# Performance work log

Measured on AMD Instinct MI355X. Metric: run time of the kernel, lower is better.

## Reference

```python
import jax, jax.numpy as jnp
import numpy as np

HEADS = 4
DIM_HEAD = 128


def setup_inputs() -> dict:
    key = jax.random.key(0)
    k1, k2, k3 = jax.random.split(key, 3)
    dim = 256
    hidden = HEADS * DIM_HEAD  # 512
    x = jax.random.normal(k1, (16, dim, 64, 64), dtype=jnp.float32)
    # 1x1 conv weights stored as [out_ch, in_ch] (kernel dims squeezed)
    w_qkv = jax.random.normal(k2, (hidden * 3, dim), dtype=jnp.float32) * (1.0 / np.sqrt(dim))
    w_out = jax.random.normal(k3, (dim, hidden), dtype=jnp.float32) * (1.0 / np.sqrt(hidden))
    b_out = jnp.zeros((dim,), dtype=jnp.float32)
    return {"x": x, "w_qkv": w_qkv, "w_out": w_out, "b_out": b_out}


def reference(x, w_qkv, w_out, b_out):
    b, c, h, w = x.shape
    n = h * w
    # 1x1 conv == per-pixel linear projection
    qkv = jnp.einsum('bchw,oc->bohw', x, w_qkv)           # [b, 3*heads*dh, h, w]
    qkv = qkv.reshape(b, 3, HEADS, DIM_HEAD, n)           # 'b (qkv heads c) h w -> qkv b heads c (h w)'
    q, k, v = qkv[:, 0], qkv[:, 1], qkv[:, 2]             # [b, heads, dh, n]
    k = jax.nn.softmax(k, axis=-1)                        # softmax over spatial positions
    context = jnp.einsum('bhdn,bhen->bhde', k, v)         # [b, heads, dh, dh]
    out = jnp.einsum('bhde,bhdn->bhen', context, q)       # [b, heads, dh, n]
    out = out.reshape(b, HEADS * DIM_HEAD, h, w)          # 'b heads c (h w) -> b (heads c) h w'
    y = jnp.einsum('bchw,oc->bohw', out, w_out) + b_out[None, :, None, None]
    return y
```

## Files before the change

kernel.cpp:

```cpp
#include <hip/hip_runtime.h>

#define BATCH 16
#define CIN   256
#define NSP   4096
#define HID   512

typedef short v8s __attribute__((ext_vector_type(8)));
typedef float v4f __attribute__((ext_vector_type(4)));

__device__ __forceinline__ unsigned short f2bf(float f) {
    union { float f; unsigned u; } a; a.f = f;
    unsigned r = a.u + 0x7fffu + ((a.u >> 16) & 1u);
    return (unsigned short)(r >> 16);
}

__device__ __forceinline__ void gld_lds16(const unsigned short* g, unsigned short* l) {
    __builtin_amdgcn_global_load_lds(
        (const __attribute__((address_space(1))) unsigned int*)g,
        (__attribute__((address_space(3))) unsigned int*)l,
        16, 0, 0);
}


__global__ __launch_bounds__(256) void k_prep(const float* __restrict__ x,
                                              const float* __restrict__ wq,
                                              unsigned short* __restrict__ xbf,
                                              unsigned short* __restrict__ xT,
                                              unsigned short* __restrict__ wbf,
                                              unsigned short* __restrict__ wqT,
                                              float* __restrict__ zacc) {
    const int bid = blockIdx.x;
    const int t = threadIdx.x;
    if (bid >= 4320) {
        zacc[(bid - 4320) * 256 + t] = 0.f;
        return;
    }
    if (bid >= 4096) {
        const int wid = bid - 4096;
        if (wid < 192) {
            const int g = wid * 256 + t;
            const float4 f0 = *(const float4*)(wq + (size_t)g * 8);
            const float4 f1 = *(const float4*)(wq + (size_t)g * 8 + 4);
            union { unsigned short s[8]; uint4 u; } p;
            p.s[0] = f2bf(f0.x); p.s[1] = f2bf(f0.y); p.s[2] = f2bf(f0.z); p.s[3] = f2bf(f0.w);
            p.s[4] = f2bf(f1.x); p.s[5] = f2bf(f1.y); p.s[6] = f2bf(f1.z); p.s[7] = f2bf(f1.w);
            *(uint4*)(wbf + (size_t)g * 8) = p.u;
            return;
        }
        __shared__ float tile[64 * 65];
        const int bb = wid - 192;
        const int u0 = (bb & 7) * 64, c0 = (bb >> 3) * 64;
        {
            const int cl = (t & 15) * 4, ul = t >> 4;
            #pragma unroll
            for (int i = 0; i < 4; i++) {
                int u = ul + i * 16;
                const float4 f = *(const float4*)(wq + (size_t)(u0 + u) * CIN + c0 + cl);
                *(float4*)(&tile[u * 65 + cl]) = f;
            }
        }
        __syncthreads();
        {
            const int ul4 = (t & 15) * 4, cl = t >> 4;
            #pragma unroll
            for (int i = 0; i < 4; i++) {
                int c = cl + i * 16;
                union { unsigned short s[4]; uint2 u; } p;
                #pragma unroll
                for (int j = 0; j < 4; j++)
                    p.s[j] = f2bf(tile[(ul4 + j) * 65 + c]);
                *(uint2*)(wqT + (size_t)(c0 + c) * HID + u0 + ul4) = p.u;
            }
        }
        return;
    }
    __shared__ float tile[64 * 65];
    const int n0 = (bid & 63) * 64, c0 = ((bid >> 6) & 3) * 64, bz = bid >> 8;
    const float* xb = x + (size_t)bz * CIN * NSP;
    {
        const int nl = (t & 15) * 4, cl = t >> 4;
        #pragma unroll
        for (int i = 0; i < 4; i++) {
            int c = cl + i * 16;
            const float4 f = *(const float4*)(xb + (size_t)(c0 + c) * NSP + n0 + nl);
            *(float4*)(&tile[c * 65 + nl]) = f;
            union { unsigned short s[4]; uint2 u; } p;
            p.s[0] = f2bf(f.x); p.s[1] = f2bf(f.y); p.s[2] = f2bf(f.z); p.s[3] = f2bf(f.w);
            *(uint2*)(xbf + ((size_t)bz * CIN + c0 + c) * NSP + n0 + nl) = p.u;
        }
    }
    __syncthreads();
    {
        const int cl4 = (t & 15) * 4, nl = t >> 4;
        #pragma unroll
        for (int i = 0; i < 4; i++) {
            int n = nl + i * 16;
            union { unsigned short s[4]; uint2 u; } p;
            #pragma unroll
            for (int j = 0; j < 4; j++)
                p.s[j] = f2bf(tile[(cl4 + j) * 65 + n]);
            *(uint2*)(xT + ((size_t)bz * NSP + n0 + n) * CIN + c0 + cl4) = p.u;
        }
    }
}

__global__ __launch_bounds__(256, 2) void k_ks(const unsigned short* __restrict__ wbf,
                                               const unsigned short* __restrict__ xT,
                                               const unsigned short* __restrict__ xbf,
                                               float* __restrict__ Sp,
                                               float* __restrict__ zacc) {
    __shared__ __align__(16) unsigned short A1s[4][64][64];
    __shared__ __align__(16) unsigned short A2s[256][64];
    __shared__ __align__(16) unsigned short Es[64][64];

    const int t = threadIdx.x;
    const int id = blockIdx.x;
    const int bz = id & 15, dblk = (id >> 4) & 7, nc = id >> 7;
    const int d0 = dblk * 64;
    const int nbase = nc * 1024;
    const int lane = t & 63, wv = t >> 6, quad = lane >> 4, l15 = lane & 15;
    const int srow8 = lane >> 3, sslot = lane & 7;
    const int scol = ((sslot - srow8) & 7) * 8;
    const int sw0 = ((quad + l15) & 7) * 8;
    const int wc = wv;

    auto STAGE_A1 = [&](int n0s) {
        #pragma unroll
        for (int i = 0; i < 8; i++) {
            const int flat = wv * 8 + i;
            const int kl = flat >> 3, rb = flat & 7;
            gld_lds16(xT + ((size_t)bz * NSP + n0s + rb * 8 + srow8) * CIN + kl * 64 + scol,
                      &A1s[kl][rb * 8][0]);
        }
    };
    auto STAGE_A2 = [&](int n0s) {
        #pragma unroll
        for (int i = 0; i < 8; i++) {
            const int rb = wv * 8 + i;
            gld_lds16(xbf + ((size_t)bz * CIN + rb * 8 + srow8) * NSP + n0s + scol,
                      &A2s[rb * 8][0]);
        }
    };

    {
        #pragma unroll
        for (int i = 0; i < 8; i++) {
            const int flat = wv * 8 + i;
            const int kk = flat >> 3, rb = flat & 7;
            gld_lds16(wbf + (size_t)(512 + d0 + rb * 8 + srow8) * CIN + kk * 64 + scol,
                      &A2s[0][0] + (kk * 64 + rb * 8) * 64);
        }
    }
    __syncthreads();
    v8s Wkf[4][4][2];
    #pragma unroll
    for (int kk = 0; kk < 4; kk++)
        #pragma unroll
        for (int ni = 0; ni < 4; ni++)
            #pragma unroll
            for (int h = 0; h < 2; h++) {
                union { v8s v; uint4 u; } rr;
                rr.u = *(const uint4*)(&A2s[0][0] +
                        (size_t)(kk * 64 + ni * 16 + l15) * 64 + (sw0 ^ (h * 32)));
                Wkf[kk][ni][h] = rr.v;
            }
    __syncthreads();

    v4f acc2[4][4];
    #pragma unroll
    for (int i = 0; i < 4; i++)
        #pragma unroll
        for (int j = 0; j < 4; j++) acc2[i][j] = (v4f)0.f;
    float za[4] = {0.f, 0.f, 0.f, 0.f};

    STAGE_A1(nbase);

    for (int nt = 0; nt < 16; nt++) {
        const int n0s = nbase + nt * 64;
        __syncthreads();
        STAGE_A2(n0s);

        v4f acc1[4];
        #pragma unroll
        for (int i = 0; i < 4; i++) acc1[i] = (v4f)0.f;

        __builtin_amdgcn_s_setprio(1);
        #pragma unroll
        for (int kk = 0; kk < 4; kk++) {
            #pragma unroll
            for (int h = 0; h < 2; h++) {
                union { v8s v; uint4 u; } rr;
                rr.u = *(const uint4*)(&A1s[kk][wv * 16 + l15][0] + (sw0 ^ (h * 32)));
                const v8s af = rr.v;
                #pragma unroll
                for (int ni = 0; ni < 4; ni++)
                    acc1[ni] = __builtin_amdgcn_mfma_f32_16x16x32_bf16(af, Wkf[kk][ni][h], acc1[ni], 0, 0, 0);
            }
        }
        __builtin_amdgcn_s_setprio(0);

        #pragma unroll
        for (int ni = 0; ni < 4; ni++) {
            const int d = ni * 16 + l15;
            union { unsigned short s[4]; uint2 u; } p;
            #pragma unroll
            for (int rr = 0; rr < 4; rr++) {
                float e = __expf(acc1[ni][rr]);
                za[ni] += e;
                p.s[rr] = f2bf(e);
            }
            const int slot = (wv * 2 + (quad >> 1) + d) & 7;
            *(uint2*)(&Es[d][slot * 8 + (quad & 1) * 4]) = p.u;
        }
        __syncthreads();
        if (nt < 15) STAGE_A1(n0s + 64);

        __builtin_amdgcn_s_setprio(1);
        #pragma unroll
        for (int kst = 0; kst < 2; kst++) {
            const int esw = sw0 ^ (kst * 32);
            v8s af[4], bfr[4];
            #pragma unroll
            for (int mi = 0; mi < 4; mi++) {
                union { v8s v; uint4 u; } rr;
                rr.u = *(const uint4*)(&A2s[wc * 64 + mi * 16 + l15][0] + esw);
                af[mi] = rr.v;
            }
            #pragma unroll
            for (int ni = 0; ni < 4; ni++) {
                union { v8s v; uint4 u; } rr;
                rr.u = *(const uint4*)(&Es[ni * 16 + l15][0] + esw);
                bfr[ni] = rr.v;
            }
            #pragma unroll
            for (int mi = 0; mi < 4; mi++)
                #pragma unroll
                for (int ni = 0; ni < 4; ni++)
                    acc2[mi][ni] = __builtin_amdgcn_mfma_f32_16x16x32_bf16(af[mi], bfr[ni], acc2[mi][ni], 0, 0, 0);
        }
        __builtin_amdgcn_s_setprio(0);
    }

    #pragma unroll
    for (int ni = 0; ni < 4; ni++) {
        float z = za[ni];
        z += __shfl_xor(z, 16);
        z += __shfl_xor(z, 32);
        if (quad == 0)
            atomicAdd(&zacc[bz * 512 + d0 + ni * 16 + l15], z);
    }

    const int bh = bz * 4 + (dblk >> 1);
    const int ch = wc >> 1;
    float* outp = Sp + ((size_t)(bh * 2 + ch) * 4 + nc) * 16384;
    #pragma unroll
    for (int ni = 0; ni < 4; ni++) {
        const int dl = (dblk & 1) * 64 + ni * 16 + l15;
        #pragma unroll
        for (int mi = 0; mi < 4; mi++) {
            const int cl = (wc & 1) * 64 + mi * 16 + quad * 4;
            *(v4f*)(outp + dl * 128 + cl) = acc2[mi][ni];
        }
    }
}

__global__ __launch_bounds__(256) void k_sred(const float* __restrict__ Sp,
                                              unsigned short* __restrict__ Sred) {
    const int qv = blockIdx.x * 256 + threadIdx.x;
    const int bh = qv >> 13, r = qv & 8191;
    const int dl = r >> 6, cq6 = r & 63;
    const int ch = cq6 >> 5, clq = cq6 & 31;
    const float* p = Sp + ((size_t)(bh * 2 + ch) * 4) * 16384 + dl * 128 + clq * 4;
    float4 s = *(const float4*)p;
    #pragma unroll
    for (int kc = 1; kc < 4; kc++) {
        const float4 f = *(const float4*)(p + (size_t)kc * 16384);
        s.x += f.x; s.y += f.y; s.z += f.z; s.w += f.w;
    }
    union { unsigned short us[4]; uint2 u; } pk;
    pk.us[0] = f2bf(s.x); pk.us[1] = f2bf(s.y); pk.us[2] = f2bf(s.z); pk.us[3] = f2bf(s.w);
    *(uint2*)(Sred + (size_t)bh * 32768 + dl * 256 + cq6 * 4) = pk.u;
}

__global__ __launch_bounds__(256) void k_redwc(const unsigned short* __restrict__ Sred,
                                               const float* __restrict__ zacc,
                                               const unsigned short* __restrict__ wbf,
                                               const float* __restrict__ w_out,
                                               unsigned short* __restrict__ Wc) {
    __shared__ unsigned short Ds[128 * 136];
    __shared__ float zinv[128];
    const int t = threadIdx.x;
    const int bh = blockIdx.x;  const int b = bh >> 2, h = bh & 3;
    const int lane = t & 63, wv = t >> 6, quad = lane >> 4, l15 = lane & 15;

    if (t < 128) zinv[t] = 1.0f / zacc[b * 512 + h * 128 + t];
    __syncthreads();

    {
        const int wm = (wv & 1) * 64, wn = (wv >> 1) * 64;
        const unsigned short* Sb = Sred + (size_t)bh * 32768;
        const unsigned short* Vb = wbf + (size_t)(1024 + h * 128) * CIN;
        v4f acc[4][4];
        #pragma unroll
        for (int i = 0; i < 4; i++)
            #pragma unroll
            for (int j = 0; j < 4; j++) acc[i][j] = (v4f)0.f;
        for (int kk = 0; kk < CIN; kk += 32) {
            v8s af[4], bfr[4];
            #pragma unroll
            for (int mi = 0; mi < 4; mi++) {
                union { v8s v; uint4 u; } rr;
                rr.u = *(const uint4*)(Sb + (size_t)(wm + mi * 16 + l15) * 256 + kk + quad * 8);
                af[mi] = rr.v;
            }
            #pragma unroll
            for (int ni = 0; ni < 4; ni++) {
                union { v8s v; uint4 u; } rr;
                rr.u = *(const uint4*)(Vb + (size_t)(wn + ni * 16 + l15) * 256 + kk + quad * 8);
                bfr[ni] = rr.v;
            }
            #pragma unroll
            for (int mi = 0; mi < 4; mi++)
                #pragma unroll
                for (int ni = 0; ni < 4; ni++)
                    acc[mi][ni] = __builtin_amdgcn_mfma_f32_16x16x32_bf16(af[mi], bfr[ni], acc[mi][ni], 0, 0, 0);
        }
        float zq[4][4];
        #pragma unroll
        for (int mi = 0; mi < 4; mi++)
            #pragma unroll
            for (int rr = 0; rr < 4; rr++)
                zq[mi][rr] = zinv[wm + mi * 16 + quad * 4 + rr];
        #pragma unroll
        for (int mi = 0; mi < 4; mi++)
            #pragma unroll
            for (int ni = 0; ni < 4; ni++)
                #pragma unroll
                for (int rr = 0; rr < 4; rr++)
                    Ds[(wm + mi * 16 + quad * 4 + rr) * 136 + wn + ni * 16 + l15] =
                        f2bf(acc[mi][ni][rr] * zq[mi][rr]);
    }
    __syncthreads();

    {
        const int wm = wv * 64;
        v4f acc[4][8];
        #pragma unroll
        for (int i = 0; i < 4; i++)
            #pragma unroll
            for (int j = 0; j < 8; j++) acc[i][j] = (v4f)0.f;
        for (int kk = 0; kk < 128; kk += 32) {
            v8s af[4], bfr[8];
            #pragma unroll
            for (int mi = 0; mi < 4; mi++) {
                int o = wm + mi * 16 + l15;
                const float* wp = w_out + (size_t)o * HID + h * 128 + kk + quad * 8;
                float4 f0 = *(const float4*)wp;
                float4 f1 = *(const float4*)(wp + 4);
                union { v8s v; unsigned short s[8]; } r;
                r.s[0] = f2bf(f0.x); r.s[1] = f2bf(f0.y); r.s[2] = f2bf(f0.z); r.s[3] = f2bf(f0.w);
                r.s[4] = f2bf(f1.x); r.s[5] = f2bf(f1.y); r.s[6] = f2bf(f1.z); r.s[7] = f2bf(f1.w);
                af[mi] = r.v;
            }
            #pragma unroll
            for (int ni = 0; ni < 8; ni++) {
                union { v8s v; uint4 u; } r;
                r.u = *(const uint4*)(&Ds[(ni * 16 + l15) * 136 + kk + quad * 8]);
                bfr[ni] = r.v;
            }
            #pragma unroll
            for (int mi = 0; mi < 4; mi++)
                #pragma unroll
                for (int ni = 0; ni < 8; ni++)
                    acc[mi][ni] = __builtin_amdgcn_mfma_f32_16x16x32_bf16(af[mi], bfr[ni], acc[mi][ni], 0, 0, 0);
        }
        #pragma unroll
        for (int ni = 0; ni < 8; ni++) {
            int d = ni * 16 + l15;
            #pragma unroll
            for (int mi = 0; mi < 4; mi++)
                #pragma unroll
                for (int rr = 0; rr < 4; rr++) {
                    int o = wm + mi * 16 + quad * 4 + rr;
                    Wc[((size_t)b * 256 + o) * HID + h * 128 + d] = f2bf(acc[mi][ni][rr]);
                }
        }
    }
}

__global__ __launch_bounds__(256) void k_chain(const unsigned short* __restrict__ Wc,
                                               const unsigned short* __restrict__ wqT,
                                               unsigned short* __restrict__ Weff) {
    __shared__ __align__(16) unsigned short As[128 * 64];
    __shared__ __align__(16) unsigned short Bs[128 * 64];
    const int t = threadIdx.x;
    const int c0 = blockIdx.x * 128, o0 = blockIdx.y * 128, bz = blockIdx.z;
    const int lane = t & 63, wv = t >> 6, quad = lane >> 4, l15 = lane & 15;
    const int wmC = (wv & 1) * 64, wnO = (wv >> 1) * 64;

    const int srow8 = lane >> 3, sslot = lane & 7;
    const int scol = ((sslot - srow8) & 7) * 8;
    const int sw0 = ((quad + l15) & 7) * 8;

    const unsigned short* Ag = wqT + (size_t)(c0 + wv * 32 + srow8) * HID + scol;
    const unsigned short* Bg = Wc + ((size_t)bz * 256 + o0 + wv * 32 + srow8) * HID + scol;
    unsigned short* Al = As + wv * 32 * 64;
    unsigned short* Bl = Bs + wv * 32 * 64;

    v4f acc[4][4];
    #pragma unroll
    for (int i = 0; i < 4; i++)
        #pragma unroll
        for (int j = 0; j < 4; j++) acc[i][j] = (v4f)0.f;

    for (int kk = 0; kk < HID; kk += 64) {
        #pragma unroll
        for (int cc = 0; cc < 4; cc++) {
            gld_lds16(Ag + (size_t)(cc * 8) * HID + kk, Al + cc * 8 * 64);
            gld_lds16(Bg + (size_t)(cc * 8) * HID + kk, Bl + cc * 8 * 64);
        }
        __syncthreads();
        #pragma unroll
        for (int h = 0; h < 2; h++) {
            const int sw = sw0 ^ (h * 32);
            v8s af[4], bfr[4];
            #pragma unroll
            for (int mi = 0; mi < 4; mi++) {
                union { v8s v; uint4 u; } rr;
                rr.u = *(const uint4*)(&As[(wmC + mi * 16 + l15) * 64 + sw]);
                af[mi] = rr.v;
            }
            #pragma unroll
            for (int ni = 0; ni < 4; ni++) {
                union { v8s v; uint4 u; } rr;
                rr.u = *(const uint4*)(&Bs[(wnO + ni * 16 + l15) * 64 + sw]);
                bfr[ni] = rr.v;
            }
            #pragma unroll
            for (int mi = 0; mi < 4; mi++)
                #pragma unroll
                for (int ni = 0; ni < 4; ni++)
                    acc[mi][ni] = __builtin_amdgcn_mfma_f32_16x16x32_bf16(af[mi], bfr[ni], acc[mi][ni], 0, 0, 0);
        }
        __syncthreads();
    }
    #pragma unroll
    for (int ni = 0; ni < 4; ni++) {
        const int o = o0 + wnO + ni * 16 + l15;
        #pragma unroll
        for (int mi = 0; mi < 4; mi++) {
            const int c = c0 + wmC + mi * 16 + quad * 4;
            union { unsigned short s[4]; uint2 u; } p;
            #pragma unroll
            for (int rr = 0; rr < 4; rr++) p.s[rr] = f2bf(acc[mi][ni][rr]);
            *(uint2*)(Weff + ((size_t)bz * 256 + o) * 256 + c) = p.u;
        }
    }
}

__global__ __launch_bounds__(256) void k_y(const unsigned short* __restrict__ Weff,
                                           const unsigned short* __restrict__ xT,
                                           const float* __restrict__ b_out,
                                           float* __restrict__ y) {
    __shared__ __align__(16) unsigned short As[128 * 64];
    __shared__ __align__(16) unsigned short Bs[128 * 64];
    const int t = threadIdx.x;
    const int o0 = blockIdx.x * 128;
    const int n0 = blockIdx.y * 128;
    const int bz = blockIdx.z;
    const int lane = t & 63, wv = t >> 6, quad = lane >> 4, l15 = lane & 15;
    const int wmN = (wv & 1) * 64, wnO = (wv >> 1) * 64;

    const int srow8 = lane >> 3, sslot = lane & 7;
    const int scol = ((sslot - srow8) & 7) * 8;
    const int sw0 = ((quad + l15) & 7) * 8;

    const unsigned short* Ag = xT + ((size_t)bz * NSP + n0 + wv * 32 + srow8) * CIN + scol;
    const unsigned short* Bg = Weff + ((size_t)bz * 256 + o0 + wv * 32 + srow8) * CIN + scol;
    unsigned short* Al = As + wv * 32 * 64;
    unsigned short* Bl = Bs + wv * 32 * 64;

    v4f acc[4][4];
    #pragma unroll
    for (int i = 0; i < 4; i++)
        #pragma unroll
        for (int j = 0; j < 4; j++) acc[i][j] = (v4f)0.f;

    for (int kk = 0; kk < CIN; kk += 64) {
        #pragma unroll
        for (int cc = 0; cc < 4; cc++) {
            gld_lds16(Ag + (size_t)(cc * 8) * CIN + kk, Al + cc * 8 * 64);
            gld_lds16(Bg + (size_t)(cc * 8) * CIN + kk, Bl + cc * 8 * 64);
        }
        __syncthreads();
        #pragma unroll
        for (int h = 0; h < 2; h++) {
            const int sw = sw0 ^ (h * 32);
            v8s af[4], bfr[4];
            #pragma unroll
            for (int mi = 0; mi < 4; mi++) {
                union { v8s v; uint4 u; } rr;
                rr.u = *(const uint4*)(&As[(wmN + mi * 16 + l15) * 64 + sw]);
                af[mi] = rr.v;
            }
            #pragma unroll
            for (int ni = 0; ni < 4; ni++) {
                union { v8s v; uint4 u; } rr;
                rr.u = *(const uint4*)(&Bs[(wnO + ni * 16 + l15) * 64 + sw]);
                bfr[ni] = rr.v;
            }
            #pragma unroll
            for (int mi = 0; mi < 4; mi++)
                #pragma unroll
                for (int ni = 0; ni < 4; ni++)
                    acc[mi][ni] = __builtin_amdgcn_mfma_f32_16x16x32_bf16(af[mi], bfr[ni], acc[mi][ni], 0, 0, 0);
        }
        __syncthreads();
    }
    #pragma unroll
    for (int ni = 0; ni < 4; ni++) {
        const int o = o0 + wnO + ni * 16 + l15;
        const float bias = b_out[o];
        #pragma unroll
        for (int mi = 0; mi < 4; mi++) {
            const int n = n0 + wmN + mi * 16 + quad * 4;
            v4f v = acc[mi][ni];
            v[0] += bias; v[1] += bias; v[2] += bias; v[3] += bias;
            *(v4f*)(y + ((size_t)bz * 256 + o) * NSP + n) = v;
        }
    }
}

extern "C" void kernel_launch(void* const* d_in, const int* in_sizes, int n_in,
                              void* d_out, int out_size, void* d_ws, size_t ws_size,
                              hipStream_t stream) {
    (void)in_sizes; (void)n_in; (void)out_size; (void)ws_size;
    const float* x     = (const float*)d_in[0];
    const float* w_qkv = (const float*)d_in[1];
    const float* w_out = (const float*)d_in[2];
    const float* b_out = (const float*)d_in[3];
    float* y = (float*)d_out;
    char* ws = (char*)d_ws;

    unsigned short* xT   = (unsigned short*)(ws);
    unsigned short* xbf  = (unsigned short*)(ws + 33554432);
    float*          Sp   = (float*)(ws + 67108864);
    float*          zacc = (float*)(ws + 100663296);
    unsigned short* Sred = (unsigned short*)(ws + 100696064);
    unsigned short* Wc   = (unsigned short*)(ws + 104890368);
    unsigned short* Weff = (unsigned short*)(ws + 109084672);
    unsigned short* wbf  = (unsigned short*)(ws + 111181824);
    unsigned short* wqT  = (unsigned short*)(ws + 111968256);

    k_prep <<<dim3(4352),       256, 0, stream>>>(x, w_qkv, xbf, xT, wbf, wqT, zacc);
    k_ks   <<<dim3(512),        256, 0, stream>>>(wbf, xT, xbf, Sp, zacc);
    k_sred <<<dim3(2048),       256, 0, stream>>>(Sp, Sred);
    k_redwc<<<dim3(64),         256, 0, stream>>>(Sred, zacc, wbf, w_out, Wc);
    k_chain<<<dim3(2, 2, 16),   256, 0, stream>>>(Wc, wqT, Weff);
    k_y    <<<dim3(2, 32, 16),  256, 0, stream>>>(Weff, xT, b_out, y);
}
```

Measured before the change: 229.4 us.

## Double-buffer LDS tiles and load x operand directly from global into registers

The k_ks kernel now double-buffers the xT tile in LDS and the exp(K) tile, prefetching the next A1 tile at the top of each iteration so one barrier per iteration suffices instead of two. The A2 (xbf) operand is no longer staged through LDS; each lane loads its MFMA fragments directly from global memory into registers. The K-weight fragments are also read straight from global memory instead of through LDS. This cuts barriers and LDS traffic, but it adds global-load latency on the critical path before the second MFMA stage, and the direct loads may be less coalesced.

```diff
diff --git a/kernel.cpp b/kernel.cpp
--- a/kernel.cpp
+++ b/kernel.cpp
@@ -109,9 +109,8 @@
                                                const unsigned short* __restrict__ xbf,
                                                float* __restrict__ Sp,
                                                float* __restrict__ zacc) {
-    __shared__ __align__(16) unsigned short A1s[4][64][64];
-    __shared__ __align__(16) unsigned short A2s[256][64];
-    __shared__ __align__(16) unsigned short Es[64][64];
+    __shared__ __align__(16) unsigned short A1s[2][4][64][64];
+    __shared__ __align__(16) unsigned short Es[2][64][64];
 
     const int t = threadIdx.x;
     const int id = blockIdx.x;
@@ -124,34 +123,16 @@
     const int sw0 = ((quad + l15) & 7) * 8;
     const int wc = wv;
 
-    auto STAGE_A1 = [&](int n0s) {
+    auto STAGE_A1 = [&](int buf, int n0s) {
         #pragma unroll
         for (int i = 0; i < 8; i++) {
             const int flat = wv * 8 + i;
             const int kl = flat >> 3, rb = flat & 7;
             gld_lds16(xT + ((size_t)bz * NSP + n0s + rb * 8 + srow8) * CIN + kl * 64 + scol,
-                      &A1s[kl][rb * 8][0]);
+                      &A1s[buf][kl][rb * 8][0]);
         }
     };
-    auto STAGE_A2 = [&](int n0s) {
-        #pragma unroll
-        for (int i = 0; i < 8; i++) {
-            const int rb = wv * 8 + i;
-            gld_lds16(xbf + ((size_t)bz * CIN + rb * 8 + srow8) * NSP + n0s + scol,
-                      &A2s[rb * 8][0]);
-        }
-    };
-
-    {
-        #pragma unroll
-        for (int i = 0; i < 8; i++) {
-            const int flat = wv * 8 + i;
-            const int kk = flat >> 3, rb = flat & 7;
-            gld_lds16(wbf + (size_t)(512 + d0 + rb * 8 + srow8) * CIN + kk * 64 + scol,
-                      &A2s[0][0] + (kk * 64 + rb * 8) * 64);
-        }
-    }
-    __syncthreads();
+
     v8s Wkf[4][4][2];
     #pragma unroll
     for (int kk = 0; kk < 4; kk++)
@@ -160,11 +141,15 @@
             #pragma unroll
             for (int h = 0; h < 2; h++) {
                 union { v8s v; uint4 u; } rr;
-                rr.u = *(const uint4*)(&A2s[0][0] +
-                        (size_t)(kk * 64 + ni * 16 + l15) * 64 + (sw0 ^ (h * 32)));
+                rr.u = *(const uint4*)(wbf + (size_t)(512 + d0 + ni * 16 + l15) * CIN +
+                                       kk * 64 + h * 32 + quad * 8);
                 Wkf[kk][ni][h] = rr.v;
             }
-    __syncthreads();
+
+    const unsigned short* g2p[4];
+    #pragma unroll
+    for (int mi = 0; mi < 4; mi++)
+        g2p[mi] = xbf + ((size_t)bz * CIN + wc * 64 + mi * 16 + l15) * NSP + quad * 8;
 
     v4f acc2[4][4];
     #pragma unroll
@@ -173,12 +158,21 @@
         for (int j = 0; j < 4; j++) acc2[i][j] = (v4f)0.f;
     float za[4] = {0.f, 0.f, 0.f, 0.f};
 
-    STAGE_A1(nbase);
-
+    STAGE_A1(0, nbase);
+    __syncthreads();
+
+    int buf = 0;
     for (int nt = 0; nt < 16; nt++) {
         const int n0s = nbase + nt * 64;
-        __syncthreads();
-        STAGE_A2(n0s);
+        if (nt < 15) STAGE_A1(buf ^ 1, n0s + 64);
+
+        v8s af20[4];
+        #pragma unroll
+        for (int mi = 0; mi < 4; mi++) {
+            union { v8s v; uint4 u; } rr;
+            rr.u = *(const uint4*)(g2p[mi] + n0s);
+            af20[mi] = rr.v;
+        }
 
         v4f acc1[4];
         #pragma unroll
@@ -190,7 +184,7 @@
             #pragma unroll
             for (int h = 0; h < 2; h++) {
                 union { v8s v; uint4 u; } rr;
-                rr.u = *(const uint4*)(&A1s[kk][wv * 16 + l15][0] + (sw0 ^ (h * 32)));
+                rr.u = *(const uint4*)(&A1s[buf][kk][wv * 16 + l15][0] + (sw0 ^ (h * 32)));
                 const v8s af = rr.v;
                 #pragma unroll
                 for (int ni = 0; ni < 4; ni++)
@@ -210,26 +204,30 @@
                 p.s[rr] = f2bf(e);
             }
             const int slot = (wv * 2 + (quad >> 1) + d) & 7;
-            *(uint2*)(&Es[d][slot * 8 + (quad & 1) * 4]) = p.u;
+            *(uint2*)(&Es[nt & 1][d][slot * 8 + (quad & 1) * 4]) = p.u;
         }
         __syncthreads();
-        if (nt < 15) STAGE_A1(n0s + 64);
 
         __builtin_amdgcn_s_setprio(1);
         #pragma unroll
         for (int kst = 0; kst < 2; kst++) {
             const int esw = sw0 ^ (kst * 32);
             v8s af[4], bfr[4];
-            #pragma unroll
-            for (int mi = 0; mi < 4; mi++) {
-                union { v8s v; uint4 u; } rr;
-                rr.u = *(const uint4*)(&A2s[wc * 64 + mi * 16 + l15][0] + esw);
-                af[mi] = rr.v;
+            if (kst == 0) {
+                #pragma unroll
+                for (int mi = 0; mi < 4; mi++) af[mi] = af20[mi];
+            } else {
+                #pragma unroll
+                for (int mi = 0; mi < 4; mi++) {
+                    union { v8s v; uint4 u; } rr;
+                    rr.u = *(const uint4*)(g2p[mi] + n0s + 32);
+                    af[mi] = rr.v;
+                }
             }
             #pragma unroll
             for (int ni = 0; ni < 4; ni++) {
                 union { v8s v; uint4 u; } rr;
-                rr.u = *(const uint4*)(&Es[ni * 16 + l15][0] + esw);
+                rr.u = *(const uint4*)(&Es[nt & 1][ni * 16 + l15][0] + esw);
                 bfr[ni] = rr.v;
             }
             #pragma unroll
@@ -239,6 +237,7 @@
                     acc2[mi][ni] = __builtin_amdgcn_mfma_f32_16x16x32_bf16(af[mi], bfr[ni], acc2[mi][ni], 0, 0, 0);
         }
         __builtin_amdgcn_s_setprio(0);
+        buf ^= 1;
     }
 
     #pragma unroll
```

After: 257.6 us. 1.12x slower.
